# Kernel optimization log

Hardware: AMD Instinct MI355X
Metric: run time of the kernel (lower is better)

Reference implementation:

```python
import jax, jax.numpy as jnp
import numpy as np

D_MODEL = 1024
NUM_HEADS = 16
D_K = D_MODEL // NUM_HEADS


def setup_inputs() -> dict:
    key = jax.random.key(0)
    ks = jax.random.split(key, 11)
    B, S = 2, 2048
    scale = 1.0 / np.sqrt(D_MODEL)
    inp = {
        "Q_in": jax.random.normal(ks[0], (B, S, D_MODEL), jnp.float32),
        "K_in": jax.random.normal(ks[1], (B, S, D_MODEL), jnp.float32),
        "V_in": jax.random.normal(ks[2], (B, S, D_MODEL), jnp.float32),
        "Wq": jax.random.normal(ks[3], (D_MODEL, D_MODEL), jnp.float32) * scale,
        "bq": jnp.zeros((D_MODEL,), jnp.float32),
        "Wk": jax.random.normal(ks[4], (D_MODEL, D_MODEL), jnp.float32) * scale,
        "bk": jnp.zeros((D_MODEL,), jnp.float32),
        "Wv": jax.random.normal(ks[5], (D_MODEL, D_MODEL), jnp.float32) * scale,
        "bv": jnp.zeros((D_MODEL,), jnp.float32),
        "Wfc": jax.random.normal(ks[6], (D_MODEL, D_MODEL), jnp.float32) * scale,
        "bfc": jnp.zeros((D_MODEL,), jnp.float32),
    }
    return inp


def _split_heads(x, B):
    # [B, S, D] -> [B, H, S, d_k]
    return x.reshape(B, -1, NUM_HEADS, D_K).transpose(0, 2, 1, 3)


def reference(Q_in, K_in, V_in, Wq, bq, Wk, bk, Wv, bv, Wfc, bfc):
    B = Q_in.shape[0]
    q = _split_heads(Q_in @ Wq + bq, B)
    k = _split_heads(K_in @ Wk + bk, B)
    v = _split_heads(V_in @ Wv + bv, B)
    # scaled dot-product attention (mask=None)
    scores = jnp.einsum("bhqd,bhkd->bhqk", q, k) / jnp.sqrt(jnp.float32(D_K))
    attn = jax.nn.softmax(scores, axis=-1)
    ctx = jnp.einsum("bhqk,bhkd->bhqd", attn, v)
    out = ctx.transpose(0, 2, 1, 3).reshape(B, -1, D_MODEL)
    out = out @ Wfc + bfc
    return out, attn
```

## Files before the change

kernel.cpp:

```cpp
#include <hip/hip_runtime.h>

typedef unsigned short u16;
typedef _Float16 f16;
typedef __attribute__((ext_vector_type(8))) f16 f16x8;
typedef __attribute__((ext_vector_type(4))) float f32x4;
typedef __attribute__((ext_vector_type(4))) u16 u16x4;
typedef __attribute__((ext_vector_type(8))) u16 u16x8;

__device__ __forceinline__ u16 f2h(float x){
  f16 h = (f16)x;
  return __builtin_bit_cast(u16, h);
}
__device__ __forceinline__ float h2f(u16 v){
  return (float)__builtin_bit_cast(f16, v);
}

__device__ __forceinline__ void stage16(const void* g, void* l){
  __builtin_amdgcn_global_load_lds(
      (const __attribute__((address_space(1))) unsigned*)g,
      (__attribute__((address_space(3))) unsigned*)l, 16, 0, 0);
}

__global__ __launch_bounds__(256) void convert_x3(
    const float* __restrict__ in0, const float* __restrict__ in1, const float* __restrict__ in2,
    u16* __restrict__ o0, u16* __restrict__ o1, u16* __restrict__ o2){
  const int b = blockIdx.x >> 12;
  const int i = (blockIdx.x & 4095) * 256 + threadIdx.x;
  const float* in = (b == 0) ? in0 : (b == 1) ? in1 : in2;
  u16* out = (b == 0) ? o0 : (b == 1) ? o1 : o2;
  f32x4 v = ((const f32x4*)in)[i];
  u16x4 h;
  #pragma unroll
  for (int j = 0; j < 4; j++) h[j] = f2h(v[j]);
  ((u16x4*)out)[i] = h;
}

__global__ __launch_bounds__(256) void transpose_w4(
    const float* __restrict__ W0, const float* __restrict__ W1,
    const float* __restrict__ W2, const float* __restrict__ W3,
    u16* __restrict__ t0, u16* __restrict__ t1, u16* __restrict__ t2, u16* __restrict__ t3){
  __shared__ float tile[64][68];
  const int z = blockIdx.z;
  const float* W = (z == 0) ? W0 : (z == 1) ? W1 : (z == 2) ? W2 : W3;
  u16* wt = (z == 0) ? t0 : (z == 1) ? t1 : (z == 2) ? t2 : t3;
  const int tid = threadIdx.x;
  const int k0 = blockIdx.y * 64, n0 = blockIdx.x * 64;
  #pragma unroll
  for (int g = 0; g < 4; g++){
    int flat4 = g * 256 + tid;
    int row = flat4 >> 4, c4 = flat4 & 15;
    f32x4 v = *(const f32x4*)&W[(size_t)(k0 + row) * 1024 + n0 + c4 * 4];
    *(f32x4*)&tile[row][c4 * 4] = v;
  }
  __syncthreads();
  const int n = tid >> 2, kc = (tid & 3) * 16;
  u16x8 o0, o1;
  #pragma unroll
  for (int j = 0; j < 8; j++){
    o0[j] = f2h(tile[kc + j][n]);
    o1[j] = f2h(tile[kc + 8 + j][n]);
  }
  u16* dst = &wt[(size_t)(n0 + n) * 1024 + k0 + kc];
  *(u16x8*)dst = o0;
  *(u16x8*)(dst + 8) = o1;
}

template<int MODE>
__device__ __forceinline__ void gemm_body(
    const u16* __restrict__ A, const u16* __restrict__ B,
    const float* __restrict__ bias,
    float* __restrict__ outF, u16* __restrict__ outH,
    int N, int K, int bx, int by)
{
  __shared__ u16 sA[128 * 32];
  __shared__ u16 sB[128 * 32];
  const int tid = threadIdx.x;
  const int wid = tid >> 6, lane = tid & 63;
  const int lm = lane & 15, lg = lane >> 4;
  const int bm = by * 128, bn = bx * 128;
  const int wrow = (wid >> 1) * 64, wcol = (wid & 1) * 64;
  const int srow = tid >> 2;
  const int skc  = (tid & 3) * 8;

  f32x4 acc[4][4] = {};

  for (int kt = 0; kt < K; kt += 32){
    {
      char* dA = (char*)sA + wid * 1024;
      char* dB = (char*)sB + wid * 1024;
      stage16(A + (size_t)(bm +      srow) * K + kt + skc, dA);
      stage16(A + (size_t)(bm + 64 + srow) * K + kt + skc, dA + 4096);
      stage16(B + (size_t)(bn +      srow) * K + kt + skc, dB);
      stage16(B + (size_t)(bn + 64 + srow) * K + kt + skc, dB + 4096);
    }
    __syncthreads();
    f16x8 af[4], bf[4];
    #pragma unroll
    for (int mf = 0; mf < 4; mf++)
      af[mf] = *(const f16x8*)&sA[(wrow + mf * 16 + lm) * 32 + lg * 8];
    #pragma unroll
    for (int nf = 0; nf < 4; nf++)
      bf[nf] = *(const f16x8*)&sB[(wcol + nf * 16 + lm) * 32 + lg * 8];
    #pragma unroll
    for (int mf = 0; mf < 4; mf++)
      #pragma unroll
      for (int nf = 0; nf < 4; nf++)
        acc[mf][nf] = __builtin_amdgcn_mfma_f32_16x16x32_f16(af[mf], bf[nf], acc[mf][nf], 0, 0, 0);
    __syncthreads();
  }

  #pragma unroll
  for (int mf = 0; mf < 4; mf++)
    #pragma unroll
    for (int nf = 0; nf < 4; nf++){
      const int n  = bn + wcol + nf * 16 + lm;
      const int mb = bm + wrow + mf * 16 + lg * 4;
      #pragma unroll
      for (int r = 0; r < 4; r++){
        const int m = mb + r;
        float v = acc[mf][nf][r] + ((MODE == 2) ? bias[m] : bias[n]);
        if constexpr (MODE == 0){
          outF[(size_t)m * N + n] = v;
        } else if constexpr (MODE == 1){
          const size_t idx = (((size_t)((m >> 11) * 16 + (n >> 6))) * 2048 + (m & 2047)) * 64 + (n & 63);
          outH[idx] = f2h(v);
        } else {
          const size_t idx = (((size_t)((n >> 11) * 16 + (m >> 6))) * 64 + (m & 63)) * 2048 + (n & 2047);
          outH[idx] = f2h(v);
        }
      }
    }
}

__global__ __launch_bounds__(256, 2) void gemm_qk(
    const u16* __restrict__ xq, const u16* __restrict__ wqt, const float* __restrict__ bq, u16* __restrict__ qh,
    const u16* __restrict__ xk, const u16* __restrict__ wkt, const float* __restrict__ bk, u16* __restrict__ kh){
  const int z = blockIdx.z;
  gemm_body<1>(z ? xk : xq, z ? wkt : wqt, z ? bk : bq, nullptr, z ? kh : qh,
               1024, 1024, blockIdx.x, blockIdx.y);
}

__global__ __launch_bounds__(256, 2) void gemm_v(
    const u16* __restrict__ wvt, const u16* __restrict__ xv, const float* __restrict__ bv, u16* __restrict__ vt){
  gemm_body<2>(wvt, xv, bv, nullptr, vt, 4096, 1024, blockIdx.x, blockIdx.y);
}

__global__ __launch_bounds__(256, 2) void gemm_fc(
    const u16* __restrict__ ctx, const u16* __restrict__ wft, const float* __restrict__ bfc, float* __restrict__ outF){
  gemm_body<0>(ctx, wft, bfc, outF, nullptr, 1024, 1024, blockIdx.x, blockIdx.y);
}

__global__ __launch_bounds__(256, 4) void attn_fused(
    const u16* __restrict__ qh_, const u16* __restrict__ kh_,
    const u16* __restrict__ vt_,
    float* __restrict__ attn_out, u16* __restrict__ ctx)
{
  constexpr int S = 2048;
  __shared__ __align__(16) u16 te[4][16][40];
  __shared__ float sred[4][16];
  __shared__ __align__(16) float cred[4][64][20];
  const int tid = threadIdx.x, wid = tid >> 6, lane = tid & 63;
  const int lm = lane & 15, lg = lane >> 4;
  const int wg = blockIdx.x;
  const int xcd = wg & 7, li = wg >> 3;
  const int bh = (xcd << 2) + (li >> 7);
  const int q0 = (li & 127) * 16;
  const size_t base = (size_t)bh * S * 64;
  const u16* Qh = qh_ + base;
  const u16* Kh = kh_ + base;
  const u16* Vt = vt_ + base;
  float* Aout = attn_out + (size_t)bh * S * S;
  const int kbase = wid * 512;

  f16x8 qb[2];
  #pragma unroll
  for (int ks = 0; ks < 2; ks++)
    qb[ks] = *(const f16x8*)(Qh + (size_t)(q0 + lm) * 64 + ks * 32 + lg * 8);

  const float SCL2 = 0.18033688011112042f;

  float part0 = 0.0f, part1 = 0.0f;
  for (int nt2 = 0; nt2 < 16; nt2++){
    const u16* kp0 = Kh + (size_t)(kbase + nt2 * 32 + lm) * 64 + lg * 8;
    const u16* kp1 = kp0 + 16 * 64;
    f16x8 k00 = *(const f16x8*)(kp0);
    f16x8 k01 = *(const f16x8*)(kp0 + 32);
    f16x8 k10 = *(const f16x8*)(kp1);
    f16x8 k11 = *(const f16x8*)(kp1 + 32);
    f32x4 c0 = {}, c1 = {};
    c0 = __builtin_amdgcn_mfma_f32_16x16x32_f16(k00, qb[0], c0, 0, 0, 0);
    c0 = __builtin_amdgcn_mfma_f32_16x16x32_f16(k01, qb[1], c0, 0, 0, 0);
    c1 = __builtin_amdgcn_mfma_f32_16x16x32_f16(k10, qb[0], c1, 0, 0, 0);
    c1 = __builtin_amdgcn_mfma_f32_16x16x32_f16(k11, qb[1], c1, 0, 0, 0);
    #pragma unroll
    for (int r = 0; r < 4; r++){
      part0 += __builtin_amdgcn_exp2f(c0[r] * SCL2);
      part1 += __builtin_amdgcn_exp2f(c1[r] * SCL2);
    }
  }
  float part = part0 + part1;
  part += __shfl_xor(part, 16);
  part += __shfl_xor(part, 32);
  if (lane < 16) sred[wid][lm] = part;
  __syncthreads();
  const float inv = 1.0f / (sred[0][lm] + sred[1][lm] + sred[2][lm] + sred[3][lm]);

  const int sq = lane >> 3;
  const int sc = (lane & 7) * 4;
  f32x4 cacc[4] = {};
  for (int nt2 = 0; nt2 < 16; nt2++){
    const int col0 = kbase + nt2 * 32;
    f16x8 vb[4];
    #pragma unroll
    for (int nf = 0; nf < 4; nf++)
      vb[nf] = *(const f16x8*)(Vt + (size_t)(nf * 16 + lm) * S + col0 + lg * 8);

    const u16* kp0 = Kh + (size_t)(col0 + lm) * 64 + lg * 8;
    const u16* kp1 = kp0 + 16 * 64;
    f16x8 k00 = *(const f16x8*)(kp0);
    f16x8 k01 = *(const f16x8*)(kp0 + 32);
    f16x8 k10 = *(const f16x8*)(kp1);
    f16x8 k11 = *(const f16x8*)(kp1 + 32);
    f32x4 c0 = {}, c1 = {};
    c0 = __builtin_amdgcn_mfma_f32_16x16x32_f16(k00, qb[0], c0, 0, 0, 0);
    c0 = __builtin_amdgcn_mfma_f32_16x16x32_f16(k01, qb[1], c0, 0, 0, 0);
    c1 = __builtin_amdgcn_mfma_f32_16x16x32_f16(k10, qb[0], c1, 0, 0, 0);
    c1 = __builtin_amdgcn_mfma_f32_16x16x32_f16(k11, qb[1], c1, 0, 0, 0);

    #pragma unroll
    for (int half = 0; half < 2; half++){
      f32x4 c = half ? c1 : c0;
      u16x4 hp;
      #pragma unroll
      for (int r = 0; r < 4; r++)
        hp[r] = f2h(__builtin_amdgcn_exp2f(c[r] * SCL2) * inv);
      *(u16x4*)&te[wid][lm][half * 16 + lg * 4] = hp;
    }
    f16x8 pa = *(const f16x8*)&te[wid][lm][lg * 8];
    #pragma unroll
    for (int nf = 0; nf < 4; nf++)
      cacc[nf] = __builtin_amdgcn_mfma_f32_16x16x32_f16(pa, vb[nf], cacc[nf], 0, 0, 0);
    #pragma unroll
    for (int i2 = 0; i2 < 2; i2++){
      const int q = i2 * 8 + sq;
      u16x4 hv = *(const u16x4*)&te[wid][q][sc];
      f32x4 av = { h2f(hv[0]), h2f(hv[1]), h2f(hv[2]), h2f(hv[3]) };
      __builtin_nontemporal_store(av, (f32x4*)(Aout + (size_t)(q0 + q) * S + col0 + sc));
    }
  }

  #pragma unroll
  for (int nf = 0; nf < 4; nf++)
    *(f32x4*)&cred[wid][nf * 16 + lm][lg * 4] = cacc[nf];
  __syncthreads();
  const int b = bh >> 4, h = bh & 15;
  const int rd = lane;
  const int rq = wid * 4;
  f32x4 s0 = *(const f32x4*)&cred[0][rd][rq];
  f32x4 s1 = *(const f32x4*)&cred[1][rd][rq];
  f32x4 s2 = *(const f32x4*)&cred[2][rd][rq];
  f32x4 s3 = *(const f32x4*)&cred[3][rd][rq];
  #pragma unroll
  for (int j = 0; j < 4; j++){
    float v = s0[j] + s1[j] + s2[j] + s3[j];
    ctx[(size_t)(b * 2048 + q0 + rq + j) * 1024 + h * 64 + rd] = f2h(v);
  }
}

extern "C" void kernel_launch(void* const* d_in, const int* in_sizes, int n_in,
                              void* d_out, int out_size, void* d_ws, size_t ws_size,
                              hipStream_t stream) {
  const float* Qi  = (const float*)d_in[0];
  const float* Ki  = (const float*)d_in[1];
  const float* Vi  = (const float*)d_in[2];
  const float* Wq  = (const float*)d_in[3];
  const float* bq  = (const float*)d_in[4];
  const float* Wk  = (const float*)d_in[5];
  const float* bk  = (const float*)d_in[6];
  const float* Wv  = (const float*)d_in[7];
  const float* bv  = (const float*)d_in[8];
  const float* Wfc = (const float*)d_in[9];
  const float* bfc = (const float*)d_in[10];

  char* w = (char*)d_ws;
  const size_t P  = 8388608;
  const size_t PW = 2097152;
  u16* xq  = (u16*)(w + 0*P);
  u16* xk  = (u16*)(w + 1*P);
  u16* xv  = (u16*)(w + 2*P);
  u16* qh  = (u16*)(w + 3*P);
  u16* kh  = (u16*)(w + 4*P);
  u16* vt  = (u16*)(w + 5*P);
  u16* ctx = (u16*)(w + 6*P);
  char* w2 = w + 7*P;
  u16* wqt = (u16*)(w2 + 0*PW);
  u16* wkt = (u16*)(w2 + 1*PW);
  u16* wvt = (u16*)(w2 + 2*PW);
  u16* wft = (u16*)(w2 + 3*PW);

  float* outp  = (float*)d_out;
  float* attnp = outp + 4194304;

  convert_x3<<<12288, 256, 0, stream>>>(Qi, Ki, Vi, xq, xk, xv);
  transpose_w4<<<dim3(16, 16, 4), 256, 0, stream>>>(Wq, Wk, Wv, Wfc, wqt, wkt, wvt, wft);

  gemm_qk<<<dim3(8, 32, 2), 256, 0, stream>>>(xq, wqt, bq, qh, xk, wkt, bk, kh);
  gemm_v<<<dim3(32, 8), 256, 0, stream>>>(wvt, xv, bv, vt);
  attn_fused<<<4096, 256, 0, stream>>>(qh, kh, vt, attnp, ctx);
  gemm_fc<<<dim3(8, 32), 256, 0, stream>>>(ctx, wft, bfc, outp);
}
```

Measured before the change: 452.4 us.

## Fuse softmax into a single pass, buffering unnormalized probabilities in LDS

The old attention kernel ran QK^T and exp twice, once for the row sums and once for the outputs. It now makes one pass. Unnormalized fp16 exponentials for each wave's 512 keys are kept in a larger LDS buffer, and the normalization is applied afterwards to both the attention-probability stores and the context accumulators. This removes half of the score MFMAs and exponentials and the second round of K loads. In exchange the kernel uses much more LDS, so occupancy drops (launch bounds go from 4 to 2). The attention writes are also issued as a burst at the end with regular rather than nontemporal stores, which reduces overlap with compute.

```diff
diff --git a/kernel.cpp b/kernel.cpp
--- a/kernel.cpp
+++ b/kernel.cpp
@@ -150,17 +150,18 @@
   gemm_body<0>(ctx, wft, bfc, outF, nullptr, 1024, 1024, blockIdx.x, blockIdx.y);
 }
 
-__global__ __launch_bounds__(256, 4) void attn_fused(
+__global__ __launch_bounds__(256, 2) void attn_fused(
     const u16* __restrict__ qh_, const u16* __restrict__ kh_,
     const u16* __restrict__ vt_,
     float* __restrict__ attn_out, u16* __restrict__ ctx)
 {
   constexpr int S = 2048;
-  __shared__ __align__(16) u16 te[4][16][40];
+  __shared__ __align__(16) char smem[4 * 16 * 520 * 2];
   __shared__ float sred[4][16];
-  __shared__ __align__(16) float cred[4][64][20];
+  __shared__ float linv[16];
   const int tid = threadIdx.x, wid = tid >> 6, lane = tid & 63;
   const int lm = lane & 15, lg = lane >> 4;
+  u16 (*pb)[520] = (u16 (*)[520])(smem + wid * (16 * 520 * 2));
   const int wg = blockIdx.x;
   const int xcd = wg & 7, li = wg >> 3;
   const int bh = (xcd << 2) + (li >> 7);
@@ -179,34 +180,7 @@
 
   const float SCL2 = 0.18033688011112042f;
 
-  float part0 = 0.0f, part1 = 0.0f;
-  for (int nt2 = 0; nt2 < 16; nt2++){
-    const u16* kp0 = Kh + (size_t)(kbase + nt2 * 32 + lm) * 64 + lg * 8;
-    const u16* kp1 = kp0 + 16 * 64;
-    f16x8 k00 = *(const f16x8*)(kp0);
-    f16x8 k01 = *(const f16x8*)(kp0 + 32);
-    f16x8 k10 = *(const f16x8*)(kp1);
-    f16x8 k11 = *(const f16x8*)(kp1 + 32);
-    f32x4 c0 = {}, c1 = {};
-    c0 = __builtin_amdgcn_mfma_f32_16x16x32_f16(k00, qb[0], c0, 0, 0, 0);
-    c0 = __builtin_amdgcn_mfma_f32_16x16x32_f16(k01, qb[1], c0, 0, 0, 0);
-    c1 = __builtin_amdgcn_mfma_f32_16x16x32_f16(k10, qb[0], c1, 0, 0, 0);
-    c1 = __builtin_amdgcn_mfma_f32_16x16x32_f16(k11, qb[1], c1, 0, 0, 0);
-    #pragma unroll
-    for (int r = 0; r < 4; r++){
-      part0 += __builtin_amdgcn_exp2f(c0[r] * SCL2);
-      part1 += __builtin_amdgcn_exp2f(c1[r] * SCL2);
-    }
-  }
-  float part = part0 + part1;
-  part += __shfl_xor(part, 16);
-  part += __shfl_xor(part, 32);
-  if (lane < 16) sred[wid][lm] = part;
-  __syncthreads();
-  const float inv = 1.0f / (sred[0][lm] + sred[1][lm] + sred[2][lm] + sred[3][lm]);
-
-  const int sq = lane >> 3;
-  const int sc = (lane & 7) * 4;
+  float part = 0.0f;
   f32x4 cacc[4] = {};
   for (int nt2 = 0; nt2 < 16; nt2++){
     const int col0 = kbase + nt2 * 32;
@@ -232,26 +206,52 @@
       f32x4 c = half ? c1 : c0;
       u16x4 hp;
       #pragma unroll
-      for (int r = 0; r < 4; r++)
-        hp[r] = f2h(__builtin_amdgcn_exp2f(c[r] * SCL2) * inv);
-      *(u16x4*)&te[wid][lm][half * 16 + lg * 4] = hp;
+      for (int r = 0; r < 4; r++){
+        float e = __builtin_amdgcn_exp2f(c[r] * SCL2);
+        part += e;
+        hp[r] = f2h(e);
+      }
+      *(u16x4*)&pb[lm][nt2 * 32 + half * 16 + lg * 4] = hp;
     }
-    f16x8 pa = *(const f16x8*)&te[wid][lm][lg * 8];
+    f16x8 pa = *(const f16x8*)&pb[lm][nt2 * 32 + lg * 8];
     #pragma unroll
     for (int nf = 0; nf < 4; nf++)
       cacc[nf] = __builtin_amdgcn_mfma_f32_16x16x32_f16(pa, vb[nf], cacc[nf], 0, 0, 0);
-    #pragma unroll
-    for (int i2 = 0; i2 < 2; i2++){
-      const int q = i2 * 8 + sq;
-      u16x4 hv = *(const u16x4*)&te[wid][q][sc];
-      f32x4 av = { h2f(hv[0]), h2f(hv[1]), h2f(hv[2]), h2f(hv[3]) };
-      __builtin_nontemporal_store(av, (f32x4*)(Aout + (size_t)(q0 + q) * S + col0 + sc));
-    }
-  }
-
-  #pragma unroll
-  for (int nf = 0; nf < 4; nf++)
-    *(f32x4*)&cred[wid][nf * 16 + lm][lg * 4] = cacc[nf];
+  }
+
+  part += __shfl_xor(part, 16);
+  part += __shfl_xor(part, 32);
+  if (lane < 16) sred[wid][lm] = part;
+  __syncthreads();
+  if (tid < 16) linv[tid] = 1.0f / (sred[0][tid] + sred[1][tid] + sred[2][tid] + sred[3][tid]);
+  __syncthreads();
+
+  #pragma unroll 4
+  for (int r = 0; r < 16; r++){
+    u16x8 hv = *(const u16x8*)&pb[r][lane * 8];
+    const float iv = linv[r];
+    f32x4 lo = { h2f(hv[0]) * iv, h2f(hv[1]) * iv, h2f(hv[2]) * iv, h2f(hv[3]) * iv };
+    f32x4 hi = { h2f(hv[4]) * iv, h2f(hv[5]) * iv, h2f(hv[6]) * iv, h2f(hv[7]) * iv };
+    float* dst = Aout + (size_t)(q0 + r) * S + kbase + lane * 8;
+    *(f32x4*)dst = lo;
+    *(f32x4*)(dst + 4) = hi;
+  }
+
+  const float myinv = linv[lg * 4 + 0];
+  (void)myinv;
+  float iv4[4];
+  #pragma unroll
+  for (int r = 0; r < 4; r++) iv4[r] = linv[lg * 4 + r];
+
+  __syncthreads();
+  float (*cred)[64][20] = (float (*)[64][20])smem;
+  #pragma unroll
+  for (int nf = 0; nf < 4; nf++){
+    f32x4 sc;
+    #pragma unroll
+    for (int r = 0; r < 4; r++) sc[r] = cacc[nf][r] * iv4[r];
+    *(f32x4*)&cred[wid][nf * 16 + lm][lg * 4] = sc;
+  }
   __syncthreads();
   const int b = bh >> 4, h = bh & 15;
   const int rd = lane;
```

After: 424.6 us. -6.2%, faster.
